# Kernel optimization log

Measured on AMD Instinct MI355X. Metric: run time of the kernel, lower is better.

## Reference

```python
import jax, jax.numpy as jnp
import numpy as np

CP = 1.0   # polynomial kernel balance (Kerv2d cp)
DP = 2     # polynomial kernel degree (Kerv2d dp)
EPS = 1e-5 # BatchNorm eps


def kerv2d(x, w, stride, padding):
    # polynomial kervolution: (patch . w + cp) ** dp, computed as conv then pointwise
    y = jax.lax.conv_general_dilated(
        x, w,
        window_strides=(stride, stride),
        padding=[(padding, padding), (padding, padding)],
        dimension_numbers=('NCHW', 'OIHW', 'NCHW'))
    return (y + CP) ** DP


def bn(x, g, b, m, v):
    # inference-mode BatchNorm2d with running stats, folded to scale/shift
    inv = g / jnp.sqrt(v + EPS)
    return x * inv[None, :, None, None] + (b - m * inv)[None, :, None, None]


def setup_inputs() -> dict:
    key = jax.random.key(0)
    ks = jax.random.split(key, 4)
    C_in, C_mid = 1024, 256  # bottleneck: 1024 -> 256 -> 256 -> 1024
    d = {
        'x':  jax.random.normal(ks[0], (128, C_in, 14, 14), jnp.float32),
        'w1': jax.random.normal(ks[1], (C_mid, C_in, 1, 1), jnp.float32) * 0.03,
        'w2': jax.random.normal(ks[2], (C_mid, C_mid, 3, 3), jnp.float32) * 0.02,
        'w3': jax.random.normal(ks[3], (C_in, C_mid, 1, 1), jnp.float32) * 0.03,
    }
    for i, c in zip((1, 2, 3), (C_mid, C_mid, C_in)):
        d[f'g{i}'] = jnp.ones((c,), jnp.float32)
        d[f'b{i}'] = jnp.zeros((c,), jnp.float32)
        d[f'm{i}'] = jnp.zeros((c,), jnp.float32)
        d[f'v{i}'] = jnp.ones((c,), jnp.float32)
    return d


def reference(x, w1, w2, w3, g1, b1, m1, v1, g2, b2, m2, v2, g3, b3, m3, v3):
    identity = x
    h = bn(kerv2d(x, w1, 1, 0), g1, b1, m1, v1)   # 1x1 kerv + BN (num_layers>34 branch)
    h = bn(kerv2d(h, w2, 1, 1), g2, b2, m2, v2)   # 3x3 kerv + BN, stride=1
    h = bn(kerv2d(h, w3, 1, 0), g3, b3, m3, v3)   # 1x1 kerv (expansion=4) + BN
    return h + identity                           # residual add (identity_downsample=None)
```

## Files before the change

### kernel.cpp

```cpp
#include <hip/hip_runtime.h>

using f32x4 = __attribute__((ext_vector_type(4))) float;
using s16x8 = __attribute__((ext_vector_type(8))) short;
using s16x4 = __attribute__((ext_vector_type(4))) short;

#define P_PIX 196
#define NPIX_ALL (128 * 196)
#define NROW  208
#define KT    32

static __device__ __forceinline__ short f2bf(float f) {
  union { float f; unsigned u; } a; a.f = f;
  unsigned u = a.u;
  u += 0x7fffu + ((u >> 16) & 1u);
  return (short)(u >> 16);
}

static __device__ __forceinline__ f32x4 mfma16(s16x8 a, s16x8 b, f32x4 c) {
  return __builtin_amdgcn_mfma_f32_16x16x32_bf16(a, b, c, 0, 0, 0);
}

static __device__ __forceinline__ void gload16(const short* g, short* l) {
  __builtin_amdgcn_global_load_lds(
      (const __attribute__((address_space(1))) unsigned int*)(g),
      (__attribute__((address_space(3))) unsigned int*)(l), 16, 0, 0);
}

static __device__ __forceinline__ const s16x8* fragp(const short* buf, int row, int l4) {
  return (const s16x8*)(buf + row * KT + ((l4 ^ ((row >> 1) & 3)) << 3));
}

static __device__ __forceinline__ void stage(const short* __restrict__ src, int srcK,
                                             int k0, short* dst, int rows, int rmax,
                                             int tid, int nthr) {
  for (int t = tid; t < rows * 4; t += nthr) {
    int r = t >> 2, c = t & 3;
    int rr = r < rmax ? r : rmax;
    int cs = c ^ ((r >> 1) & 3);
    gload16(src + (size_t)rr * srcK + k0 + cs * 8, dst + t * 8);
  }
}


__global__ void k_prep(const float* __restrict__ w1, const float* __restrict__ w2,
                       const float* __restrict__ w3,
                       const float* g1, const float* b1, const float* m1, const float* v1,
                       const float* g2, const float* b2, const float* m2, const float* v2,
                       const float* g3, const float* b3, const float* m3, const float* v3,
                       float* bn, short* W1b, short* W2t, short* W3b) {
  int i = blockIdx.x * 256 + threadIdx.x;
  if (i < 65536) {
    f32x4 v = *(const f32x4*)(w1 + i * 4);
    s16x4 o;
    o[0] = f2bf(v[0]); o[1] = f2bf(v[1]); o[2] = f2bf(v[2]); o[3] = f2bf(v[3]);
    *(s16x4*)(W1b + i * 4) = o;
  } else if (i < 131072) {
    int q = i - 65536;
    f32x4 v = *(const f32x4*)(w3 + q * 4);
    s16x4 o;
    o[0] = f2bf(v[0]); o[1] = f2bf(v[1]); o[2] = f2bf(v[2]); o[3] = f2bf(v[3]);
    *(s16x4*)(W3b + q * 4) = o;
  } else if (i < 278528) {
    int q = (i - 131072) * 4;
    s16x4 o;
    #pragma unroll
    for (int k = 0; k < 4; ++k) {
      int idx = q + k;
      int s = idx >> 16, rem = idx & 65535;
      int co = rem >> 8, ci = rem & 255;
      o[k] = f2bf(w2[(co * 256 + ci) * 9 + s]);
    }
    *(s16x4*)(W2t + q) = o;
  } else if (i < 280064) {
    int t = i - 278528;
    if (t < 256) {
      float inv = g1[t] * rsqrtf(v1[t] + 1e-5f);
      bn[t] = inv; bn[256 + t] = b1[t] - m1[t] * inv;
    } else if (t < 512) {
      int c = t - 256;
      float inv = g2[c] * rsqrtf(v2[c] + 1e-5f);
      bn[512 + c] = inv; bn[768 + c] = b2[c] - m2[c] * inv;
    } else {
      int c = t - 512;
      float inv = g3[c] * rsqrtf(v3[c] + 1e-5f);
      bn[1024 + c] = inv; bn[2048 + c] = b3[c] - m3[c] * inv;
    }
  }
}


__global__ __launch_bounds__(256) void k_layer1(
    const float* __restrict__ x, const short* __restrict__ W1b,
    const float* __restrict__ bnbuf, short* __restrict__ H1) {
  __shared__ __align__(16) short lB[2][128 * KT];
  const int tid = threadIdx.x;
  const int vb = (blockIdx.x & 7) * 64 + (blockIdx.x >> 3);
  const int n = vb >> 2, mb = (vb >> 1) & 1, jh = vb & 1;
  const int lane = tid & 63, wave = tid >> 6;
  const int l15 = lane & 15, l4 = lane >> 4;

  if (jh == 1 && tid < 96) {
    int bb = tid / 48, idx = tid % 48;
    s16x8 z = {0,0,0,0,0,0,0,0};
    *(s16x8*)(&lB[bb][100 * KT + idx * 8]) = z;
  }

  const float* xs = x + (size_t)n * 1024 * P_PIX;
  const short* Asrc = W1b + (size_t)(mb * 128) * 1024;

  const int npg = jh ? 25 : 28;
  const int pgbase = jh ? 24 : 0;
  const bool act = tid < npg * 8;
  const int pg = pgbase + (act ? tid % npg : 0);
  const int kg = act ? tid / npg : 0;
  const int lrow0 = pg * 4 - jh * 96;

  f32x4 rX[4], rY[4];
  auto loadx = [&](int kt, f32x4* r) {
    if (!act) return;
    const float* sp = xs + (size_t)(kt * 32 + kg * 4) * P_PIX + pg * 4;
    r[0] = *(const f32x4*)sp;
    r[1] = *(const f32x4*)(sp + P_PIX);
    r[2] = *(const f32x4*)(sp + 2 * P_PIX);
    r[3] = *(const f32x4*)(sp + 3 * P_PIX);
  };
  auto cvtw = [&](const f32x4* r, short* buf) {
    if (!act) return;
    int chunk = kg >> 1, inner = (kg & 1) * 4;
    #pragma unroll
    for (int q = 0; q < 4; ++q) {
      int lr = lrow0 + q;
      s16x4 w;
      w[0] = f2bf(r[0][q]); w[1] = f2bf(r[1][q]);
      w[2] = f2bf(r[2][q]); w[3] = f2bf(r[3][q]);
      *(s16x4*)(buf + lr * KT + ((chunk ^ ((lr >> 1) & 3)) << 3) + inner) = w;
    }
  };
  auto LA = [&](int kt, int m) -> s16x8 {
    return *(const s16x8*)(Asrc + (size_t)(wave * 32 + m * 16 + l15) * 1024 + kt * 32 + l4 * 8);
  };

  f32x4 acc[2][7];
  f32x4 zero = {0.f, 0.f, 0.f, 0.f};
  #pragma unroll
  for (int m = 0; m < 2; ++m)
    #pragma unroll
    for (int jj = 0; jj < 7; ++jj) acc[m][jj] = zero;

  loadx(0, rX);
  loadx(1, rY);
  cvtw(rX, lB[0]);
  s16x8 a0c = LA(0, 0), a1c = LA(0, 1);
  __syncthreads();

  auto body = [&](int kt, f32x4* rNext, f32x4* rFill) {
    s16x8 a0n = a0c, a1n = a1c;
    if (kt + 1 < 32) { a0n = LA(kt + 1, 0); a1n = LA(kt + 1, 1); }
    if (kt + 2 < 32) loadx(kt + 2, rFill);
    const short* B = lB[kt & 1];
    #pragma unroll
    for (int jj = 0; jj < 7; ++jj) {
      s16x8 bfr = *fragp(B, jj * 16 + l15, l4);
      acc[0][jj] = mfma16(a0c, bfr, acc[0][jj]);
      acc[1][jj] = mfma16(a1c, bfr, acc[1][jj]);
    }
    if (kt + 1 < 32) cvtw(rNext, lB[(kt + 1) & 1]);
    __syncthreads();
    a0c = a0n; a1c = a1n;
  };

  for (int kt = 0; kt < 32; kt += 2) {
    body(kt, rY, rX);
    body(kt + 1, rX, rY);
  }

  short* Hn = H1 + (size_t)n * P_PIX * 256;
  #pragma unroll
  for (int m = 0; m < 2; ++m) {
    int co = mb * 128 + wave * 32 + m * 16 + l4 * 4;
    f32x4 sc = *(const f32x4*)(bnbuf + co);
    f32x4 sh = *(const f32x4*)(bnbuf + 256 + co);
    #pragma unroll
    for (int jj = 0; jj < 7; ++jj) {
      if (jh && jj == 0) continue;
      int p = (jh * 6 + jj) * 16 + l15;
      if (p < P_PIX) {
        s16x4 o;
        #pragma unroll
        for (int i = 0; i < 4; ++i) {
          float y = acc[m][jj][i] + 1.0f;
          o[i] = f2bf(y * y * sc[i] + sh[i]);
        }
        *(s16x4*)(Hn + p * 256 + co) = o;
      }
    }
  }
}


__global__ __launch_bounds__(512) void k_layer2(
    const short* __restrict__ H1, const short* __restrict__ W2t,
    const float* __restrict__ bnbuf, short* __restrict__ H2) {
  __shared__ __align__(16) short lB[197 * 256];
  const int tid = threadIdx.x;
  const int vb = (blockIdx.x & 7) * 32 + (blockIdx.x >> 3);
  const int n = vb >> 1, jh = vb & 1;
  const int lane = tid & 63, wave = tid >> 6;
  const int l15 = lane & 15, l4 = lane >> 4;

  const short* Bsrc = H1 + (size_t)n * P_PIX * 256;
  for (int t = tid; t < 6272; t += 512) {
    int row = t >> 5, pc = t & 31;
    int lc = pc ^ (row & 7);
    gload16(Bsrc + row * 256 + lc * 8, lB + t * 8);
  }
  if (tid < 32) {
    s16x8 z = {0,0,0,0,0,0,0,0};
    *(s16x8*)(&lB[196 * 256 + tid * 8]) = z;
  }

  int vm[7];
  #pragma unroll
  for (int jj = 0; jj < 7; ++jj) {
    int p = (jh * 6 + jj) * 16 + l15;
    int m = 0;
    if (p < P_PIX) {
      int h = p / 14, w = p % 14;
      m = 2 | 16;
      if (h >= 1)  m |= 1;
      if (h < 13)  m |= 4;
      if (w >= 1)  m |= 8;
      if (w < 13)  m |= 32;
    }
    vm[jj] = m;
  }

  f32x4 acc[2][7];
  f32x4 zero = {0.f, 0.f, 0.f, 0.f};
  #pragma unroll
  for (int m = 0; m < 2; ++m)
    #pragma unroll
    for (int jj = 0; jj < 7; ++jj) acc[m][jj] = zero;

  auto LA = [&](int kt, int s, int m) -> s16x8 {
    return *(const s16x8*)(W2t +
        (size_t)((s * 256 + wave * 32 + m * 16 + l15) * 256) + kt * 32 + l4 * 8);
  };

  __syncthreads();

  s16x8 aC0 = LA(0, 0, 0), aC1 = LA(0, 0, 1);
  for (int kt = 0; kt < 8; ++kt) {
    const int lcb = kt << 2;
    #pragma unroll
    for (int s = 0; s < 9; ++s) {
      s16x8 aN0 = aC0, aN1 = aC1;
      const int s1 = (s == 8) ? 0 : s + 1;
      const int kt1 = (s == 8) ? kt + 1 : kt;
      if (kt1 < 8) { aN0 = LA(kt1, s1, 0); aN1 = LA(kt1, s1, 1); }
      const int dy = s / 3, dx = s % 3;
      const int doff = (dy - 1) * 14 + (dx - 1);
      #pragma unroll
      for (int jj = 0; jj < 7; ++jj) {
        int p = (jh * 6 + jj) * 16 + l15;
        bool valid = ((vm[jj] >> dy) & 1) && ((vm[jj] >> (3 + dx)) & 1);
        int row = valid ? (p + doff) : 196;
        int pc = (lcb | l4) ^ (row & 7);
        s16x8 bfr = *(const s16x8*)(lB + row * 256 + (pc << 3));
        acc[0][jj] = mfma16(aC0, bfr, acc[0][jj]);
        acc[1][jj] = mfma16(aC1, bfr, acc[1][jj]);
      }
      aC0 = aN0; aC1 = aN1;
    }
  }

  short* Hn = H2 + (size_t)n * P_PIX * 256;
  #pragma unroll
  for (int m = 0; m < 2; ++m) {
    int co = wave * 32 + m * 16 + l4 * 4;
    f32x4 sc = *(const f32x4*)(bnbuf + 512 + co);
    f32x4 sh = *(const f32x4*)(bnbuf + 768 + co);
    #pragma unroll
    for (int jj = 0; jj < 7; ++jj) {
      if (jh && jj == 0) continue;
      int p = (jh * 6 + jj) * 16 + l15;
      if (p < P_PIX) {
        s16x4 o;
        #pragma unroll
        for (int i = 0; i < 4; ++i) {
          float y = acc[m][jj][i] + 1.0f;
          o[i] = f2bf(y * y * sc[i] + sh[i]);
        }
        *(s16x4*)(Hn + p * 256 + co) = o;
      }
    }
  }
}


__global__ __launch_bounds__(256) void k_layer3(
    const short* __restrict__ H2, const short* __restrict__ W3b,
    const float* __restrict__ bnbuf, const float* __restrict__ x,
    float* __restrict__ out) {
  __shared__ __align__(16) char smem[27136];
  short* const lB0 = (short*)smem;
  short* const lB1 = lB0 + NROW * KT;
  float* const eb = (float*)smem;

  const int tid = threadIdx.x;
  const int vb = (blockIdx.x & 7) * 256 + (blockIdx.x >> 3);
  const int n = vb >> 4, mb = vb & 15;
  const int lane = tid & 63, wave = tid >> 6;
  const int l15 = lane & 15, l4 = lane >> 4;

  const short* Asrc = W3b + (size_t)(mb * 64) * 256;
  const short* Bsrc = H2 + (size_t)n * P_PIX * 256;

  f32x4 acc[13];
  f32x4 zero = {0.f, 0.f, 0.f, 0.f};
  #pragma unroll
  for (int j = 0; j < 13; ++j) acc[j] = zero;

  auto LA = [&](int kt) -> s16x8 {
    return *(const s16x8*)(Asrc + (size_t)(wave * 16 + l15) * 256 + kt * 32 + l4 * 8);
  };

  stage(Bsrc, 256, 0, lB0, NROW, P_PIX - 1, tid, 256);
  s16x8 ac = LA(0);
  __syncthreads();

  for (int kt = 0; kt < 8; ++kt) {
    s16x8 an = ac;
    if (kt + 1 < 8) an = LA(kt + 1);
    if (kt < 7)
      stage(Bsrc, 256, (kt + 1) * 32, ((kt + 1) & 1) ? lB1 : lB0, NROW, P_PIX - 1, tid, 256);
    const short* B = (kt & 1) ? lB1 : lB0;
    #pragma unroll
    for (int j = 0; j < 13; ++j) {
      s16x8 bfr = *fragp(B, j * 16 + l15, l4);
      acc[j] = mfma16(ac, bfr, acc[j]);
    }
    __syncthreads();
    ac = an;
  }

  const int co_r = tid >> 3;
  const int pcb  = tid & 7;
  #pragma unroll
  for (int h = 0; h < 2; ++h) {
    __syncthreads();
    if ((wave >> 1) == h) {
      const int co_l = (wave & 1) * 16 + l4 * 4;
      #pragma unroll
      for (int j = 0; j < 13; ++j) {
        const int p = j * 16 + l15;
        #pragma unroll
        for (int i = 0; i < 4; ++i)
          eb[(co_l + i) * 212 + p] = acc[j][i];
      }
    }
    __syncthreads();
    const int co_g = mb * 64 + h * 32 + co_r;
    const float scv = bnbuf[1024 + co_g];
    const float shv = bnbuf[2048 + co_g];
    const size_t rowbase = ((size_t)(n * 1024 + co_g)) * P_PIX;
    #pragma unroll
    for (int pass = 0; pass < 7; ++pass) {
      const int pc = pcb + pass * 8;
      if (pc < 49) {
        f32x4 v = *(const f32x4*)(eb + co_r * 212 + pc * 4);
        const size_t idx = rowbase + pc * 4;
        f32x4 xv = *(const f32x4*)(x + idx);
        f32x4 o;
        #pragma unroll
        for (int k = 0; k < 4; ++k) {
          float y = v[k] + 1.0f;
          o[k] = y * y * scv + shv + xv[k];
        }
        *(f32x4*)(out + idx) = o;
      }
    }
  }
}


extern "C" void kernel_launch(void* const* d_in, const int* in_sizes, int n_in,
                              void* d_out, int out_size, void* d_ws, size_t ws_size,
                              hipStream_t stream) {
  (void)in_sizes; (void)n_in; (void)out_size; (void)ws_size;
  const float* x  = (const float*)d_in[0];
  const float* w1 = (const float*)d_in[1];
  const float* w2 = (const float*)d_in[2];
  const float* w3 = (const float*)d_in[3];
  const float* g1 = (const float*)d_in[4];
  const float* b1 = (const float*)d_in[5];
  const float* m1 = (const float*)d_in[6];
  const float* v1 = (const float*)d_in[7];
  const float* g2 = (const float*)d_in[8];
  const float* b2 = (const float*)d_in[9];
  const float* m2 = (const float*)d_in[10];
  const float* v2 = (const float*)d_in[11];
  const float* g3 = (const float*)d_in[12];
  const float* b3 = (const float*)d_in[13];
  const float* m3 = (const float*)d_in[14];
  const float* v3 = (const float*)d_in[15];

  char* ws = (char*)d_ws;
  short* W1b   = (short*)(ws + 0);
  short* W2t   = (short*)(ws + 524288);
  short* W3b   = (short*)(ws + 1703936);
  float* bnbuf = (float*)(ws + 2228224);
  short* H1    = (short*)(ws + 2240512);
  short* H2    = (short*)(ws + 15085568);

  k_prep<<<1094, 256, 0, stream>>>(w1, w2, w3,
                                   g1, b1, m1, v1, g2, b2, m2, v2, g3, b3, m3, v3,
                                   bnbuf, W1b, W2t, W3b);
  k_layer1<<<512, 256, 0, stream>>>(x, W1b, bnbuf, H1);
  k_layer2<<<256, 512, 0, stream>>>(H1, W2t, bnbuf, H2);
  k_layer3<<<2048, 256, 0, stream>>>(H2, W3b, bnbuf, x, (float*)d_out);
}
```

Before: 138.0 us.

## Stage full-K activation tile in LDS for layer1 and split by pixel quarter

```diff
diff --git a/kernel.cpp b/kernel.cpp
--- a/kernel.cpp
+++ b/kernel.cpp
@@ -89,109 +89,94 @@
 }
 
 
-__global__ __launch_bounds__(256) void k_layer1(
+__global__ __launch_bounds__(512) void k_layer1(
     const float* __restrict__ x, const short* __restrict__ W1b,
     const float* __restrict__ bnbuf, short* __restrict__ H1) {
-  __shared__ __align__(16) short lB[2][128 * KT];
+  __shared__ __align__(16) short lB[64 * 1024];
   const int tid = threadIdx.x;
   const int vb = (blockIdx.x & 7) * 64 + (blockIdx.x >> 3);
-  const int n = vb >> 2, mb = (vb >> 1) & 1, jh = vb & 1;
+  const int n = vb >> 2, pq = vb & 3;
   const int lane = tid & 63, wave = tid >> 6;
   const int l15 = lane & 15, l4 = lane >> 4;
-
-  if (jh == 1 && tid < 96) {
-    int bb = tid / 48, idx = tid % 48;
-    s16x8 z = {0,0,0,0,0,0,0,0};
-    *(s16x8*)(&lB[bb][100 * KT + idx * 8]) = z;
-  }
+  const int j0 = (pq == 0) ? 0 : 1 + 3 * pq;
+  const int nj = (pq == 0) ? 4 : 3;
+  const int row0 = j0 * 16;
 
   const float* xs = x + (size_t)n * 1024 * P_PIX;
-  const short* Asrc = W1b + (size_t)(mb * 128) * 1024;
-
-  const int npg = jh ? 25 : 28;
-  const int pgbase = jh ? 24 : 0;
-  const bool act = tid < npg * 8;
-  const int pg = pgbase + (act ? tid % npg : 0);
-  const int kg = act ? tid / npg : 0;
-  const int lrow0 = pg * 4 - jh * 96;
-
-  f32x4 rX[4], rY[4];
-  auto loadx = [&](int kt, f32x4* r) {
-    if (!act) return;
-    const float* sp = xs + (size_t)(kt * 32 + kg * 4) * P_PIX + pg * 4;
-    r[0] = *(const f32x4*)sp;
-    r[1] = *(const f32x4*)(sp + P_PIX);
-    r[2] = *(const f32x4*)(sp + 2 * P_PIX);
-    r[3] = *(const f32x4*)(sp + 3 * P_PIX);
+  #pragma unroll
+  for (int it = 0; it < 8; ++it) {
+    int idx = it * 512 + tid;
+    int pgr = idx & 15;
+    int cg  = idx >> 4;
+    int p0 = row0 + pgr * 4;
+    if (p0 > 192) p0 = 192;
+    const float* sp = xs + (size_t)(cg * 4) * P_PIX + p0;
+    f32x4 v0 = *(const f32x4*)sp;
+    f32x4 v1 = *(const f32x4*)(sp + P_PIX);
+    f32x4 v2 = *(const f32x4*)(sp + 2 * P_PIX);
+    f32x4 v3 = *(const f32x4*)(sp + 3 * P_PIX);
+    #pragma unroll
+    for (int q = 0; q < 4; ++q) {
+      int lr = pgr * 4 + q;
+      s16x4 w;
+      w[0] = f2bf(v0[q]); w[1] = f2bf(v1[q]);
+      w[2] = f2bf(v2[q]); w[3] = f2bf(v3[q]);
+      int ch = (cg >> 1) ^ (lr & 7);
+      *(s16x4*)(lB + lr * 1024 + ch * 8 + (cg & 1) * 4) = w;
+    }
+  }
+
+  f32x4 acc[2][4];
+  f32x4 zero = {0.f, 0.f, 0.f, 0.f};
+  #pragma unroll
+  for (int m = 0; m < 2; ++m)
+    #pragma unroll
+    for (int jj = 0; jj < 4; ++jj) acc[m][jj] = zero;
+
+  const short* Asrc = W1b + (size_t)(wave * 32 + l15) * 1024 + l4 * 8;
+  auto LA = [&](int kt, int m) -> s16x8 {
+    return *(const s16x8*)(Asrc + (size_t)(m * 16) * 1024 + kt * 32);
   };
-  auto cvtw = [&](const f32x4* r, short* buf) {
-    if (!act) return;
-    int chunk = kg >> 1, inner = (kg & 1) * 4;
-    #pragma unroll
-    for (int q = 0; q < 4; ++q) {
-      int lr = lrow0 + q;
-      s16x4 w;
-      w[0] = f2bf(r[0][q]); w[1] = f2bf(r[1][q]);
-      w[2] = f2bf(r[2][q]); w[3] = f2bf(r[3][q]);
-      *(s16x4*)(buf + lr * KT + ((chunk ^ ((lr >> 1) & 3)) << 3) + inner) = w;
-    }
-  };
-  auto LA = [&](int kt, int m) -> s16x8 {
-    return *(const s16x8*)(Asrc + (size_t)(wave * 32 + m * 16 + l15) * 1024 + kt * 32 + l4 * 8);
-  };
-
-  f32x4 acc[2][7];
-  f32x4 zero = {0.f, 0.f, 0.f, 0.f};
-  #pragma unroll
-  for (int m = 0; m < 2; ++m)
-    #pragma unroll
-    for (int jj = 0; jj < 7; ++jj) acc[m][jj] = zero;
-
-  loadx(0, rX);
-  loadx(1, rY);
-  cvtw(rX, lB[0]);
+
+  __syncthreads();
+
   s16x8 a0c = LA(0, 0), a1c = LA(0, 1);
-  __syncthreads();
-
-  auto body = [&](int kt, f32x4* rNext, f32x4* rFill) {
+  for (int kt = 0; kt < 32; ++kt) {
     s16x8 a0n = a0c, a1n = a1c;
     if (kt + 1 < 32) { a0n = LA(kt + 1, 0); a1n = LA(kt + 1, 1); }
-    if (kt + 2 < 32) loadx(kt + 2, rFill);
-    const short* B = lB[kt & 1];
-    #pragma unroll
-    for (int jj = 0; jj < 7; ++jj) {
-      s16x8 bfr = *fragp(B, jj * 16 + l15, l4);
-      acc[0][jj] = mfma16(a0c, bfr, acc[0][jj]);
-      acc[1][jj] = mfma16(a1c, bfr, acc[1][jj]);
-    }
-    if (kt + 1 < 32) cvtw(rNext, lB[(kt + 1) & 1]);
-    __syncthreads();
+    const int cb = kt << 2;
+    #pragma unroll
+    for (int jj = 0; jj < 4; ++jj) {
+      if (jj < nj) {
+        int row = jj * 16 + l15;
+        int ch = (cb | l4) ^ (row & 7);
+        s16x8 bfr = *(const s16x8*)(lB + row * 1024 + (ch << 3));
+        acc[0][jj] = mfma16(a0c, bfr, acc[0][jj]);
+        acc[1][jj] = mfma16(a1c, bfr, acc[1][jj]);
+      }
+    }
     a0c = a0n; a1c = a1n;
-  };
-
-  for (int kt = 0; kt < 32; kt += 2) {
-    body(kt, rY, rX);
-    body(kt + 1, rX, rY);
   }
 
   short* Hn = H1 + (size_t)n * P_PIX * 256;
   #pragma unroll
   for (int m = 0; m < 2; ++m) {
-    int co = mb * 128 + wave * 32 + m * 16 + l4 * 4;
+    int co = wave * 32 + m * 16 + l4 * 4;
     f32x4 sc = *(const f32x4*)(bnbuf + co);
     f32x4 sh = *(const f32x4*)(bnbuf + 256 + co);
     #pragma unroll
-    for (int jj = 0; jj < 7; ++jj) {
-      if (jh && jj == 0) continue;
-      int p = (jh * 6 + jj) * 16 + l15;
-      if (p < P_PIX) {
-        s16x4 o;
-        #pragma unroll
-        for (int i = 0; i < 4; ++i) {
-          float y = acc[m][jj][i] + 1.0f;
-          o[i] = f2bf(y * y * sc[i] + sh[i]);
+    for (int jj = 0; jj < 4; ++jj) {
+      if (jj < nj) {
+        int p = (j0 + jj) * 16 + l15;
+        if (p < P_PIX) {
+          s16x4 o;
+          #pragma unroll
+          for (int i = 0; i < 4; ++i) {
+            float y = acc[m][jj][i] + 1.0f;
+            o[i] = f2bf(y * y * sc[i] + sh[i]);
+          }
+          *(s16x4*)(Hn + p * 256 + co) = o;
         }
-        *(s16x4*)(Hn + p * 256 + co) = o;
       }
     }
   }
@@ -416,7 +401,7 @@
   k_prep<<<1094, 256, 0, stream>>>(w1, w2, w3,
                                    g1, b1, m1, v1, g2, b2, m2, v2, g3, b3, m3, v3,
                                    bnbuf, W1b, W2t, W3b);
-  k_layer1<<<512, 256, 0, stream>>>(x, W1b, bnbuf, H1);
+  k_layer1<<<512, 512, 0, stream>>>(x, W1b, bnbuf, H1);
   k_layer2<<<256, 512, 0, stream>>>(H1, W2t, bnbuf, H2);
   k_layer3<<<2048, 256, 0, stream>>>(H2, W3b, bnbuf, x, (float*)d_out);
 }
```

Result: slower. 150.8 us (+9.3%).

## Pre-transpose input to bf16 pixel-major and stage full K in LDS for layer1

Applied to the files above, without the earlier changes.

```diff
diff --git a/kernel.cpp b/kernel.cpp
--- a/kernel.cpp
+++ b/kernel.cpp
@@ -89,6 +89,101 @@
 }
 
 
+__global__ __launch_bounds__(256) void k_xpose(const float* __restrict__ x,
+                                               short* __restrict__ xb) {
+  const int n = blockIdx.x >> 4, cig = blockIdx.x & 15;
+  const int l = threadIdx.x & 63, w = threadIdx.x >> 6;
+  const float* xs = x + ((size_t)n * 1024 + cig * 64 + l) * P_PIX;
+  short* xd = xb + (size_t)n * P_PIX * 1024 + cig * 64 + l;
+  const int ni = (w == 0) ? 13 : 12;
+  for (int i = 0; i < ni; ++i) {
+    int pc = w + i * 4;
+    f32x4 v = *(const f32x4*)(xs + pc * 4);
+    #pragma unroll
+    for (int q = 0; q < 4; ++q)
+      xd[(size_t)(pc * 4 + q) * 1024] = f2bf(v[q]);
+  }
+}
+
+
+__global__ __launch_bounds__(512) void k_layer1x(
+    const short* __restrict__ xb, const short* __restrict__ W1b,
+    const float* __restrict__ bnbuf, short* __restrict__ H1) {
+  __shared__ __align__(16) short lB[64 * 1024];
+  const int tid = threadIdx.x;
+  const int vb = (blockIdx.x & 7) * 64 + (blockIdx.x >> 3);
+  const int n = vb >> 2, pq = vb & 3;
+  const int lane = tid & 63, wave = tid >> 6;
+  const int l15 = lane & 15, l4 = lane >> 4;
+  const int j0 = (pq == 0) ? 0 : 1 + 3 * pq;
+  const int nj = (pq == 0) ? 4 : 3;
+  const int row0 = j0 * 16;
+
+  const short* xbn = xb + (size_t)n * P_PIX * 1024;
+  const int ntask = nj * 16 * 128;
+  for (int t = tid; t < ntask; t += 512) {
+    int row = t >> 7, pc = t & 127;
+    int lc = pc ^ (row & 7);
+    int gr = row0 + row; if (gr > 195) gr = 195;
+    gload16(xbn + (size_t)gr * 1024 + lc * 8, lB + t * 8);
+  }
+
+  f32x4 acc[2][4];
+  f32x4 zero = {0.f, 0.f, 0.f, 0.f};
+  #pragma unroll
+  for (int m = 0; m < 2; ++m)
+    #pragma unroll
+    for (int jj = 0; jj < 4; ++jj) acc[m][jj] = zero;
+
+  const short* Asrc = W1b + (size_t)(wave * 32 + l15) * 1024 + l4 * 8;
+  auto LA = [&](int kt, int m) -> s16x8 {
+    return *(const s16x8*)(Asrc + (size_t)(m * 16) * 1024 + kt * 32);
+  };
+
+  __syncthreads();
+
+  s16x8 a0c = LA(0, 0), a1c = LA(0, 1);
+  for (int kt = 0; kt < 32; ++kt) {
+    s16x8 a0n = a0c, a1n = a1c;
+    if (kt + 1 < 32) { a0n = LA(kt + 1, 0); a1n = LA(kt + 1, 1); }
+    #pragma unroll
+    for (int jj = 0; jj < 4; ++jj) {
+      if (jj < nj) {
+        int row = jj * 16 + l15;
+        int ch = ((kt << 2) | l4) ^ (row & 7);
+        s16x8 bfr = *(const s16x8*)(lB + row * 1024 + (ch << 3));
+        acc[0][jj] = mfma16(a0c, bfr, acc[0][jj]);
+        acc[1][jj] = mfma16(a1c, bfr, acc[1][jj]);
+      }
+    }
+    a0c = a0n; a1c = a1n;
+  }
+
+  short* Hn = H1 + (size_t)n * P_PIX * 256;
+  #pragma unroll
+  for (int m = 0; m < 2; ++m) {
+    int co = wave * 32 + m * 16 + l4 * 4;
+    f32x4 sc = *(const f32x4*)(bnbuf + co);
+    f32x4 sh = *(const f32x4*)(bnbuf + 256 + co);
+    #pragma unroll
+    for (int jj = 0; jj < 4; ++jj) {
+      if (jj < nj) {
+        int p = (j0 + jj) * 16 + l15;
+        if (p < P_PIX) {
+          s16x4 o;
+          #pragma unroll
+          for (int i = 0; i < 4; ++i) {
+            float y = acc[m][jj][i] + 1.0f;
+            o[i] = f2bf(y * y * sc[i] + sh[i]);
+          }
+          *(s16x4*)(Hn + p * 256 + co) = o;
+        }
+      }
+    }
+  }
+}
+
+
 __global__ __launch_bounds__(256) void k_layer1(
     const float* __restrict__ x, const short* __restrict__ W1b,
     const float* __restrict__ bnbuf, short* __restrict__ H1) {
@@ -387,7 +482,7 @@
 extern "C" void kernel_launch(void* const* d_in, const int* in_sizes, int n_in,
                               void* d_out, int out_size, void* d_ws, size_t ws_size,
                               hipStream_t stream) {
-  (void)in_sizes; (void)n_in; (void)out_size; (void)ws_size;
+  (void)in_sizes; (void)n_in; (void)out_size;
   const float* x  = (const float*)d_in[0];
   const float* w1 = (const float*)d_in[1];
   const float* w2 = (const float*)d_in[2];
@@ -412,11 +507,18 @@
   float* bnbuf = (float*)(ws + 2228224);
   short* H1    = (short*)(ws + 2240512);
   short* H2    = (short*)(ws + 15085568);
+  short* xb    = (short*)(ws + 15085568);
+  const bool big = ws_size >= 66465792ULL;
 
   k_prep<<<1094, 256, 0, stream>>>(w1, w2, w3,
                                    g1, b1, m1, v1, g2, b2, m2, v2, g3, b3, m3, v3,
                                    bnbuf, W1b, W2t, W3b);
-  k_layer1<<<512, 256, 0, stream>>>(x, W1b, bnbuf, H1);
+  if (big) {
+    k_xpose<<<2048, 256, 0, stream>>>(x, xb);
+    k_layer1x<<<512, 512, 0, stream>>>(xb, W1b, bnbuf, H1);
+  } else {
+    k_layer1<<<512, 256, 0, stream>>>(x, W1b, bnbuf, H1);
+  }
   k_layer2<<<256, 512, 0, stream>>>(H1, W2t, bnbuf, H2);
   k_layer3<<<2048, 256, 0, stream>>>(H2, W3b, bnbuf, x, (float*)d_out);
 }
```

New measurement: 175.6 us. +27.2%, slower.
